# Performance work log

Hardware: AMD Instinct MI355X
Metric: run time of the kernel (lower is better)

The kernel has to match this reference:

```python
import jax, jax.numpy as jnp
import numpy as np

D_MODEL = 1024
NUM_HEADS = 16
DK = D_MODEL // NUM_HEADS


def setup_inputs() -> dict:
    key = jax.random.key(0)
    ks = jax.random.split(key, 9)
    s = 1.0 / np.sqrt(D_MODEL)
    x = jax.random.normal(ks[0], (4, 2048, D_MODEL), dtype=jnp.float32)
    Wq = jax.random.uniform(ks[1], (D_MODEL, D_MODEL), jnp.float32, -s, s)
    bq = jax.random.uniform(ks[2], (D_MODEL,), jnp.float32, -s, s)
    Wk = jax.random.uniform(ks[3], (D_MODEL, D_MODEL), jnp.float32, -s, s)
    bk = jax.random.uniform(ks[4], (D_MODEL,), jnp.float32, -s, s)
    Wv = jax.random.uniform(ks[5], (D_MODEL, D_MODEL), jnp.float32, -s, s)
    bv = jax.random.uniform(ks[6], (D_MODEL,), jnp.float32, -s, s)
    Wo = jax.random.uniform(ks[7], (D_MODEL, D_MODEL), jnp.float32, -s, s)
    bo = jax.random.uniform(ks[8], (D_MODEL,), jnp.float32, -s, s)
    return {"x": x, "Wq": Wq, "bq": bq, "Wk": Wk, "bk": bk,
            "Wv": Wv, "bv": bv, "Wo": Wo, "bo": bo}


def reference(x, Wq, bq, Wk, bk, Wv, bv, Wo, bo):
    B, S, _ = x.shape
    H, dk = NUM_HEADS, DK
    # QKV projections (nn.Linear: x @ W.T + b), split into heads -> [B,H,S,dk]
    q = (x @ Wq.T + bq).reshape(B, S, H, dk).transpose(0, 2, 1, 3)
    k = (x @ Wk.T + bk).reshape(B, S, H, dk).transpose(0, 2, 1, 3)
    v = (x @ Wv.T + bv).reshape(B, S, H, dk).transpose(0, 2, 1, 3)
    scores = jnp.einsum('bhqd,bhkd->bhqk', q, k) / jnp.sqrt(jnp.asarray(dk, x.dtype))
    causal = jnp.triu(jnp.ones((S, S), dtype=bool), k=1)  # True above diagonal
    scores = jnp.where(causal[None, None], -jnp.inf, scores)
    attn = jax.nn.softmax(scores, axis=-1)  # dropout p=0.0 -> identity
    out = jnp.einsum('bhqk,bhkd->bhqd', attn, v)
    out = out.transpose(0, 2, 1, 3).reshape(B, S, H * dk)
    return out @ Wo.T + bo
```

## Files before the change

### kernel.cpp

```cpp
#include <hip/hip_runtime.h>
#include <stdint.h>


#define D_MODEL 1024
#define NHEAD   16
#define DK      64
#define BATCH   4
#define SEQ     2048
#define MTOT    (BATCH*SEQ)

typedef unsigned short u16;
typedef unsigned int   u32;
typedef __bf16    bf16x8  __attribute__((ext_vector_type(8)));
typedef float     floatx4 __attribute__((ext_vector_type(4)));
typedef __fp16    fp16x2  __attribute__((ext_vector_type(2)));
typedef _Float16  half4_t __attribute__((ext_vector_type(4)));
typedef _Float16  half8_t __attribute__((ext_vector_type(8)));

__device__ __forceinline__ u16 f2bf(float f){
  union { float f; u32 u; } c; c.f = f;
  u32 x = c.u;
  x += 0x7fffu + ((x >> 16) & 1u);
  return (u16)(x >> 16);
}
__device__ __forceinline__ u32 pkh(float a, float b){
  union { fp16x2 h; u32 u; } c; c.h = __builtin_amdgcn_cvt_pkrtz(a, b); return c.u;
}
__device__ __forceinline__ uint4 pk8(const float* __restrict__ p){
  uint4 a = *(const uint4*)p;
  uint4 b = *(const uint4*)(p + 4);
  uint4 r;
  r.x = __builtin_amdgcn_perm(a.y, a.x, 0x07060302);
  r.y = __builtin_amdgcn_perm(a.w, a.z, 0x07060302);
  r.z = __builtin_amdgcn_perm(b.y, b.x, 0x07060302);
  r.w = __builtin_amdgcn_perm(b.w, b.z, 0x07060302);
  return r;
}
__device__ __forceinline__ void gload16(const void* g, void* l){
  __builtin_amdgcn_global_load_lds(
      (const __attribute__((address_space(1))) u32*)g,
      (__attribute__((address_space(3))) u32*)l, 16, 0, 0);
}

__global__ __launch_bounds__(256)
void conv4(const float* __restrict__ x,  u16* __restrict__ xb,
           const float* __restrict__ wq, const float* __restrict__ wk,
           const float* __restrict__ wv, u16* __restrict__ wb)
{
  const int b = blockIdx.x;
  const float* s; u16* d; size_t base;
  if (b < 4096)      { s = x;  d = xb;            base = (size_t)b * 2048; }
  else if (b < 4608) { s = wq; d = wb;            base = (size_t)(b-4096) * 2048; }
  else if (b < 5120) { s = wk; d = wb + (1u<<20); base = (size_t)(b-4608) * 2048; }
  else               { s = wv; d = wb + (2u<<20); base = (size_t)(b-5120) * 2048; }
  const size_t i = base + (size_t)threadIdx.x * 8;
  *(uint4*)(d + i) = pk8(s + i);
}

__global__ __launch_bounds__(256)
void conv1(const float* __restrict__ s, u16* __restrict__ d)
{
  const size_t i = ((size_t)blockIdx.x * 256 + threadIdx.x) * 8;
  *(uint4*)(d + i) = pk8(s + i);
}

template<int MODE>
__global__ __launch_bounds__(128, 2)
void gemm_bt(const u16* __restrict__ A, const u16* __restrict__ W,
             const float* __restrict__ bias, void* __restrict__ outv,
             float scale)
{
  __shared__ __align__(16) u16 As[128*32];
  __shared__ __align__(16) u16 Bs[64*32];

  const int t    = threadIdx.x;
  const int m0   = blockIdx.x * 128;
  const int n0   = blockIdx.y * 64;
  const int wid  = t >> 6, lane = t & 63;
  const int wr   = wid;
  const int quad = lane >> 4, l15 = lane & 15;

  const int rS = t >> 2;
  const int kS = (t & 3) * 8;

  const u16* Ap = A + (size_t)(m0 + rS)*D_MODEL + kS;
  const u16* Wp = W + (size_t)(n0 + rS)*D_MODEL + kS;

  floatx4 acc[4][4] = {};

  for (int k0 = 0; k0 < D_MODEL; k0 += 32) {
    __syncthreads();
    gload16(Ap + k0,               (char*)As + t*16);
    gload16(Ap + k0 + 32*D_MODEL,  (char*)As + 2048 + t*16);
    gload16(Ap + k0 + 64*D_MODEL,  (char*)As + 4096 + t*16);
    gload16(Ap + k0 + 96*D_MODEL,  (char*)As + 6144 + t*16);
    gload16(Wp + k0,               (char*)Bs + t*16);
    gload16(Wp + k0 + 32*D_MODEL,  (char*)Bs + 2048 + t*16);
    __syncthreads();

    bf16x8 af[4], bf[4];
#pragma unroll
    for (int i = 0; i < 4; ++i) {
      af[i] = *(const bf16x8*)&As[(wr*64 + i*16 + l15)*32 + quad*8];
      bf[i] = *(const bf16x8*)&Bs[(i*16 + l15)*32 + quad*8];
    }
#pragma unroll
    for (int mi = 0; mi < 4; ++mi)
#pragma unroll
      for (int nj = 0; nj < 4; ++nj) {
        if (MODE == 2)
          acc[mi][nj] = __builtin_amdgcn_mfma_f32_16x16x32_bf16(af[mi], bf[nj], acc[mi][nj], 0, 0, 0);
        else
          acc[mi][nj] = __builtin_amdgcn_mfma_f32_16x16x32_bf16(bf[nj], af[mi], acc[mi][nj], 0, 0, 0);
      }
  }

  if (MODE != 2) {
#pragma unroll
    for (int nj = 0; nj < 4; ++nj) {
      const int nb = n0 + nj*16 + quad*4;
      const float4 b4 = *(const float4*)(bias + nb);
#pragma unroll
      for (int mi = 0; mi < 4; ++mi) {
        const int m = m0 + wr*64 + mi*16 + l15;
        floatx4 d = acc[mi][nj];
        const float v0 = (d[0]+b4.x)*scale, v1 = (d[1]+b4.y)*scale;
        const float v2 = (d[2]+b4.z)*scale, v3 = (d[3]+b4.w)*scale;
        if (MODE == 0) {
          float4 s4 = make_float4(v0, v1, v2, v3);
          *(float4*)((float*)outv + (size_t)m*D_MODEL + nb) = s4;
        } else {
          const int b = m >> 11, s = m & 2047, h = nb >> 6, dd = nb & 63;
          u16* dst = (u16*)outv + ((((size_t)b*NHEAD + h)*SEQ + s) << 6) + dd;
          *(uint2*)dst = make_uint2(pkh(v0, v1), pkh(v2, v3));
        }
      }
    }
  } else {
#pragma unroll
    for (int nj = 0; nj < 4; ++nj) {
      const int n  = n0 + nj*16 + l15;
      const float bvv = bias[n];
      const int h = n >> 6, dd = n & 63;
#pragma unroll
      for (int mi = 0; mi < 4; ++mi) {
        const int mb = m0 + wr*64 + mi*16 + quad*4;
        const int b = mb >> 11, s = mb & 2047;
        floatx4 d = acc[mi][nj];
        u16* dst = (u16*)outv + (((size_t)b*NHEAD + h)*DK + dd)*SEQ + s;
        *(uint2*)dst = make_uint2(pkh(d[0]+bvv, d[1]+bvv), pkh(d[2]+bvv, d[3]+bvv));
      }
    }
  }
}

__global__ __launch_bounds__(256, 6)
void attn_fwd(const _Float16* __restrict__ Q, const _Float16* __restrict__ K,
              const _Float16* __restrict__ Vt, u16* __restrict__ O)
{
  __shared__ __align__(16) _Float16 Ks[64][72];
  __shared__ __align__(16) _Float16 Vs[64][72];

  const int bh   = blockIdx.x;
  const int pid  = blockIdx.y;
  const int t    = threadIdx.x;
  const int w    = t >> 6, lane = t & 63;
  const int quad = lane >> 4, l15 = lane & 15;
  const int sr = t >> 3, sc8 = (t & 7) * 8;
  const _Float16* Kb = K  + (size_t)bh * SEQ * DK;
  const _Float16* Vb = Vt + (size_t)bh * DK * SEQ;

#pragma unroll 1
  for (int item = 0; item < 2; ++item) {
    const int rblk = item ? pid : (SEQ/64 - 1 - pid);
    const int r0   = rblk * 64;
    const int qb   = r0 + w * 16;
    const int query = qb + l15;

    half8_t qf[2];
    {
      const _Float16* Qp = Q + ((size_t)bh * SEQ + query) * DK + quad * 8;
      qf[0] = *(const half8_t*)(Qp);
      qf[1] = *(const half8_t*)(Qp + 32);
    }

    float mrow = -1e30f, lpart = 0.f;
    floatx4 o[4] = {};

    const int jend = r0 + 64;
    for (int j0 = 0; j0 < jend; j0 += 64) {
      __syncthreads();
      *(uint4*)&Ks[sr     ][sc8] = *(const uint4*)(Kb + (size_t)(j0 + sr     )*DK + sc8);
      *(uint4*)&Ks[sr + 32][sc8] = *(const uint4*)(Kb + (size_t)(j0 + sr + 32)*DK + sc8);
      *(uint4*)&Vs[sr     ][sc8] = *(const uint4*)(Vb + (size_t)(sr     )*SEQ + j0 + sc8);
      *(uint4*)&Vs[sr + 32][sc8] = *(const uint4*)(Vb + (size_t)(sr + 32)*SEQ + j0 + sc8);
      __syncthreads();
      if (j0 > qb + 15) continue;
      const int ktmax = ((qb + 15 - j0) >> 4) + 1;

      floatx4 st[4];
#pragma unroll
      for (int kt = 0; kt < 4; ++kt) {
        if (kt < ktmax) {
          half8_t a0 = *(const half8_t*)&Ks[kt*16 + l15][quad*8];
          half8_t a1 = *(const half8_t*)&Ks[kt*16 + l15][32 + quad*8];
          floatx4 s = {};
          s = __builtin_amdgcn_mfma_f32_16x16x32_f16(a0, qf[0], s, 0, 0, 0);
          s = __builtin_amdgcn_mfma_f32_16x16x32_f16(a1, qf[1], s, 0, 0, 0);
          st[kt] = s;
        }
      }
#pragma unroll
      for (int kt = 0; kt < 4; ++kt) {
        if (kt < ktmax && j0 + kt*16 + 15 > qb) {
#pragma unroll
          for (int r = 0; r < 4; ++r)
            if (j0 + kt*16 + quad*4 + r > query) st[kt][r] = -1e30f;
        }
      }
      float m0 = -1e30f;
#pragma unroll
      for (int kt = 0; kt < 4; ++kt)
        if (kt < ktmax)
          m0 = fmaxf(m0, fmaxf(fmaxf(st[kt][0], st[kt][1]), fmaxf(st[kt][2], st[kt][3])));
      m0 = fmaxf(m0, __shfl_xor(m0, 16));
      m0 = fmaxf(m0, __shfl_xor(m0, 32));
      const float mn    = fmaxf(mrow, m0);
      const float alpha = exp2f(mrow - mn);
      mrow = mn;
      lpart *= alpha;
      half4_t pf[4];
#pragma unroll
      for (int kt = 0; kt < 4; ++kt) {
        if (kt < ktmax) {
          const float p0 = exp2f(st[kt][0] - mn), p1 = exp2f(st[kt][1] - mn);
          const float p2 = exp2f(st[kt][2] - mn), p3 = exp2f(st[kt][3] - mn);
          lpart += (p0 + p1) + (p2 + p3);
          union { half4_t h; uint2 u; } pc;
          pc.u = make_uint2(pkh(p0, p1), pkh(p2, p3));
          pf[kt] = pc.h;
        }
      }
#pragma unroll
      for (int dt = 0; dt < 4; ++dt) {
        o[dt][0] *= alpha; o[dt][1] *= alpha; o[dt][2] *= alpha; o[dt][3] *= alpha;
      }
#pragma unroll
      for (int dt = 0; dt < 4; ++dt)
#pragma unroll
        for (int kt = 0; kt < 4; ++kt) {
          if (kt < ktmax) {
            half4_t vf = *(const half4_t*)&Vs[dt*16 + l15][kt*16 + quad*4];
            o[dt] = __builtin_amdgcn_mfma_f32_16x16x16f16(vf, pf[kt], o[dt], 0, 0, 0);
          }
        }
    }

    float l = lpart;
    l += __shfl_xor(l, 16);
    l += __shfl_xor(l, 32);
    const float inv = 1.0f / l;
    const int b = bh >> 4, h = bh & 15;
    u16* Op = O + ((size_t)(b * SEQ + query)) * D_MODEL + h * DK + quad * 4;
#pragma unroll
    for (int dt = 0; dt < 4; ++dt) {
      u32 lo = ((u32)f2bf(o[dt][1] * inv) << 16) | f2bf(o[dt][0] * inv);
      u32 hi = ((u32)f2bf(o[dt][3] * inv) << 16) | f2bf(o[dt][2] * inv);
      *(uint2*)(Op + dt * 16) = make_uint2(lo, hi);
    }
  }
}

extern "C" void kernel_launch(void* const* d_in, const int* in_sizes, int n_in,
                              void* d_out, int out_size, void* d_ws, size_t ws_size,
                              hipStream_t stream)
{
  const float* x  = (const float*)d_in[0];
  const float* Wq = (const float*)d_in[1];
  const float* bq = (const float*)d_in[2];
  const float* Wk = (const float*)d_in[3];
  const float* bk = (const float*)d_in[4];
  const float* Wv = (const float*)d_in[5];
  const float* bv = (const float*)d_in[6];
  const float* Wo = (const float*)d_in[7];
  const float* bo = (const float*)d_in[8];

  const size_t tsz = (size_t)MTOT * D_MODEL;
  u16* Qw  = (u16*)d_ws;
  u16* Kw  = Qw + tsz;
  u16* Vtw = Kw + tsz;
  u16* S3  = Vtw + tsz;
  u16* WB  = (u16*)d_out;

  conv4<<<4096 + 3*512, 256, 0, stream>>>(x, S3, Wq, Wk, Wv, WB);

  dim3 gg(MTOT/128, D_MODEL/64);
  gemm_bt<1><<<gg, 128, 0, stream>>>(S3, WB,            bq, Qw,  0.18033688f);
  gemm_bt<1><<<gg, 128, 0, stream>>>(S3, WB + (1u<<20), bk, Kw,  1.0f);
  gemm_bt<2><<<gg, 128, 0, stream>>>(S3, WB + (2u<<20), bv, Vtw, 1.0f);

  attn_fwd<<<dim3(BATCH*NHEAD, SEQ/128), 256, 0, stream>>>(
      (const _Float16*)Qw, (const _Float16*)Kw, (const _Float16*)Vtw, S3);

  conv1<<<512, 256, 0, stream>>>(Wo, Qw);
  gemm_bt<0><<<gg, 128, 0, stream>>>(S3, Qw, bo, d_out, 1.0f);
}
```

Before: 322.6 us.

## Process both causal query blocks in one pass over shared K/V tiles

```diff
diff --git a/kernel.cpp b/kernel.cpp
--- a/kernel.cpp
+++ b/kernel.cpp
@@ -154,7 +154,72 @@
   }
 }
 
-__global__ __launch_bounds__(256, 6)
+__device__ __forceinline__ void attn_tile(
+    const _Float16 (*Ks)[72], const _Float16 (*Vs)[72],
+    int j0, int qb, int query, int quad, int l15,
+    const half8_t* qf, float& mrow, float& lpart, floatx4* o)
+{
+  const int ktmax = ((qb + 15 - j0) >> 4) + 1;
+
+  floatx4 st[4];
+#pragma unroll
+  for (int kt = 0; kt < 4; ++kt) {
+    if (kt < ktmax) {
+      half8_t a0 = *(const half8_t*)&Ks[kt*16 + l15][quad*8];
+      half8_t a1 = *(const half8_t*)&Ks[kt*16 + l15][32 + quad*8];
+      floatx4 s = {};
+      s = __builtin_amdgcn_mfma_f32_16x16x32_f16(a0, qf[0], s, 0, 0, 0);
+      s = __builtin_amdgcn_mfma_f32_16x16x32_f16(a1, qf[1], s, 0, 0, 0);
+      st[kt] = s;
+    }
+  }
+#pragma unroll
+  for (int kt = 0; kt < 4; ++kt) {
+    if (kt < ktmax && j0 + kt*16 + 15 > qb) {
+#pragma unroll
+      for (int r = 0; r < 4; ++r)
+        if (j0 + kt*16 + quad*4 + r > query) st[kt][r] = -1e30f;
+    }
+  }
+  float m0 = -1e30f;
+#pragma unroll
+  for (int kt = 0; kt < 4; ++kt)
+    if (kt < ktmax)
+      m0 = fmaxf(m0, fmaxf(fmaxf(st[kt][0], st[kt][1]), fmaxf(st[kt][2], st[kt][3])));
+  m0 = fmaxf(m0, __shfl_xor(m0, 16));
+  m0 = fmaxf(m0, __shfl_xor(m0, 32));
+  const float mn    = fmaxf(mrow, m0);
+  const float alpha = exp2f(mrow - mn);
+  mrow = mn;
+  lpart *= alpha;
+  half4_t pf[4];
+#pragma unroll
+  for (int kt = 0; kt < 4; ++kt) {
+    if (kt < ktmax) {
+      const float p0 = exp2f(st[kt][0] - mn), p1 = exp2f(st[kt][1] - mn);
+      const float p2 = exp2f(st[kt][2] - mn), p3 = exp2f(st[kt][3] - mn);
+      lpart += (p0 + p1) + (p2 + p3);
+      union { half4_t h; uint2 u; } pc;
+      pc.u = make_uint2(pkh(p0, p1), pkh(p2, p3));
+      pf[kt] = pc.h;
+    }
+  }
+#pragma unroll
+  for (int dt = 0; dt < 4; ++dt) {
+    o[dt][0] *= alpha; o[dt][1] *= alpha; o[dt][2] *= alpha; o[dt][3] *= alpha;
+  }
+#pragma unroll
+  for (int dt = 0; dt < 4; ++dt)
+#pragma unroll
+    for (int kt = 0; kt < 4; ++kt) {
+      if (kt < ktmax) {
+        half4_t vf = *(const half4_t*)&Vs[dt*16 + l15][kt*16 + quad*4];
+        o[dt] = __builtin_amdgcn_mfma_f32_16x16x16f16(vf, pf[kt], o[dt], 0, 0, 0);
+      }
+    }
+}
+
+__global__ __launch_bounds__(256, 4)
 void attn_fwd(const _Float16* __restrict__ Q, const _Float16* __restrict__ K,
               const _Float16* __restrict__ Vt, u16* __restrict__ O)
 {
@@ -170,102 +235,65 @@
   const _Float16* Kb = K  + (size_t)bh * SEQ * DK;
   const _Float16* Vb = Vt + (size_t)bh * DK * SEQ;
 
+  const int rblk0 = 31 - pid;
+  const int rblk1 = pid;
+  const int qb0 = rblk0*64 + w*16, q0 = qb0 + l15;
+  const int qb1 = rblk1*64 + w*16, q1 = qb1 + l15;
+
+  half8_t qf0[2], qf1[2];
+  {
+    const _Float16* Qp0 = Q + ((size_t)bh * SEQ + q0) * DK + quad * 8;
+    qf0[0] = *(const half8_t*)(Qp0);
+    qf0[1] = *(const half8_t*)(Qp0 + 32);
+    const _Float16* Qp1 = Q + ((size_t)bh * SEQ + q1) * DK + quad * 8;
+    qf1[0] = *(const half8_t*)(Qp1);
+    qf1[1] = *(const half8_t*)(Qp1 + 32);
+  }
+
+  float mrow0 = -1e30f, lpart0 = 0.f;
+  float mrow1 = -1e30f, lpart1 = 0.f;
+  floatx4 o0[4] = {};
+  floatx4 o1[4] = {};
+
+  const int jend = rblk0*64 + 64;
 #pragma unroll 1
-  for (int item = 0; item < 2; ++item) {
-    const int rblk = item ? pid : (SEQ/64 - 1 - pid);
-    const int r0   = rblk * 64;
-    const int qb   = r0 + w * 16;
-    const int query = qb + l15;
-
-    half8_t qf[2];
-    {
-      const _Float16* Qp = Q + ((size_t)bh * SEQ + query) * DK + quad * 8;
-      qf[0] = *(const half8_t*)(Qp);
-      qf[1] = *(const half8_t*)(Qp + 32);
-    }
-
-    float mrow = -1e30f, lpart = 0.f;
-    floatx4 o[4] = {};
-
-    const int jend = r0 + 64;
-    for (int j0 = 0; j0 < jend; j0 += 64) {
-      __syncthreads();
-      *(uint4*)&Ks[sr     ][sc8] = *(const uint4*)(Kb + (size_t)(j0 + sr     )*DK + sc8);
-      *(uint4*)&Ks[sr + 32][sc8] = *(const uint4*)(Kb + (size_t)(j0 + sr + 32)*DK + sc8);
-      *(uint4*)&Vs[sr     ][sc8] = *(const uint4*)(Vb + (size_t)(sr     )*SEQ + j0 + sc8);
-      *(uint4*)&Vs[sr + 32][sc8] = *(const uint4*)(Vb + (size_t)(sr + 32)*SEQ + j0 + sc8);
-      __syncthreads();
-      if (j0 > qb + 15) continue;
-      const int ktmax = ((qb + 15 - j0) >> 4) + 1;
-
-      floatx4 st[4];
-#pragma unroll
-      for (int kt = 0; kt < 4; ++kt) {
-        if (kt < ktmax) {
-          half8_t a0 = *(const half8_t*)&Ks[kt*16 + l15][quad*8];
-          half8_t a1 = *(const half8_t*)&Ks[kt*16 + l15][32 + quad*8];
-          floatx4 s = {};
-          s = __builtin_amdgcn_mfma_f32_16x16x32_f16(a0, qf[0], s, 0, 0, 0);
-          s = __builtin_amdgcn_mfma_f32_16x16x32_f16(a1, qf[1], s, 0, 0, 0);
-          st[kt] = s;
-        }
-      }
-#pragma unroll
-      for (int kt = 0; kt < 4; ++kt) {
-        if (kt < ktmax && j0 + kt*16 + 15 > qb) {
-#pragma unroll
-          for (int r = 0; r < 4; ++r)
-            if (j0 + kt*16 + quad*4 + r > query) st[kt][r] = -1e30f;
-        }
-      }
-      float m0 = -1e30f;
-#pragma unroll
-      for (int kt = 0; kt < 4; ++kt)
-        if (kt < ktmax)
-          m0 = fmaxf(m0, fmaxf(fmaxf(st[kt][0], st[kt][1]), fmaxf(st[kt][2], st[kt][3])));
-      m0 = fmaxf(m0, __shfl_xor(m0, 16));
-      m0 = fmaxf(m0, __shfl_xor(m0, 32));
-      const float mn    = fmaxf(mrow, m0);
-      const float alpha = exp2f(mrow - mn);
-      mrow = mn;
-      lpart *= alpha;
-      half4_t pf[4];
-#pragma unroll
-      for (int kt = 0; kt < 4; ++kt) {
-        if (kt < ktmax) {
-          const float p0 = exp2f(st[kt][0] - mn), p1 = exp2f(st[kt][1] - mn);
-          const float p2 = exp2f(st[kt][2] - mn), p3 = exp2f(st[kt][3] - mn);
-          lpart += (p0 + p1) + (p2 + p3);
-          union { half4_t h; uint2 u; } pc;
-          pc.u = make_uint2(pkh(p0, p1), pkh(p2, p3));
-          pf[kt] = pc.h;
-        }
-      }
-#pragma unroll
-      for (int dt = 0; dt < 4; ++dt) {
-        o[dt][0] *= alpha; o[dt][1] *= alpha; o[dt][2] *= alpha; o[dt][3] *= alpha;
-      }
-#pragma unroll
-      for (int dt = 0; dt < 4; ++dt)
-#pragma unroll
-        for (int kt = 0; kt < 4; ++kt) {
-          if (kt < ktmax) {
-            half4_t vf = *(const half4_t*)&Vs[dt*16 + l15][kt*16 + quad*4];
-            o[dt] = __builtin_amdgcn_mfma_f32_16x16x16f16(vf, pf[kt], o[dt], 0, 0, 0);
-          }
-        }
-    }
-
-    float l = lpart;
+  for (int j0 = 0; j0 < jend; j0 += 64) {
+    __syncthreads();
+    *(uint4*)&Ks[sr     ][sc8] = *(const uint4*)(Kb + (size_t)(j0 + sr     )*DK + sc8);
+    *(uint4*)&Ks[sr + 32][sc8] = *(const uint4*)(Kb + (size_t)(j0 + sr + 32)*DK + sc8);
+    *(uint4*)&Vs[sr     ][sc8] = *(const uint4*)(Vb + (size_t)(sr     )*SEQ + j0 + sc8);
+    *(uint4*)&Vs[sr + 32][sc8] = *(const uint4*)(Vb + (size_t)(sr + 32)*SEQ + j0 + sc8);
+    __syncthreads();
+    if (j0 <= qb0 + 15)
+      attn_tile(Ks, Vs, j0, qb0, q0, quad, l15, qf0, mrow0, lpart0, o0);
+    if (j0 <= qb1 + 15)
+      attn_tile(Ks, Vs, j0, qb1, q1, quad, l15, qf1, mrow1, lpart1, o1);
+  }
+
+  const int b = bh >> 4, h = bh & 15;
+  {
+    float l = lpart0;
     l += __shfl_xor(l, 16);
     l += __shfl_xor(l, 32);
     const float inv = 1.0f / l;
-    const int b = bh >> 4, h = bh & 15;
-    u16* Op = O + ((size_t)(b * SEQ + query)) * D_MODEL + h * DK + quad * 4;
+    u16* Op = O + ((size_t)(b * SEQ + q0)) * D_MODEL + h * DK + quad * 4;
 #pragma unroll
     for (int dt = 0; dt < 4; ++dt) {
-      u32 lo = ((u32)f2bf(o[dt][1] * inv) << 16) | f2bf(o[dt][0] * inv);
-      u32 hi = ((u32)f2bf(o[dt][3] * inv) << 16) | f2bf(o[dt][2] * inv);
+      u32 lo = ((u32)f2bf(o0[dt][1] * inv) << 16) | f2bf(o0[dt][0] * inv);
+      u32 hi = ((u32)f2bf(o0[dt][3] * inv) << 16) | f2bf(o0[dt][2] * inv);
+      *(uint2*)(Op + dt * 16) = make_uint2(lo, hi);
+    }
+  }
+  {
+    float l = lpart1;
+    l += __shfl_xor(l, 16);
+    l += __shfl_xor(l, 32);
+    const float inv = 1.0f / l;
+    u16* Op = O + ((size_t)(b * SEQ + q1)) * D_MODEL + h * DK + quad * 4;
+#pragma unroll
+    for (int dt = 0; dt < 4; ++dt) {
+      u32 lo = ((u32)f2bf(o1[dt][1] * inv) << 16) | f2bf(o1[dt][0] * inv);
+      u32 hi = ((u32)f2bf(o1[dt][3] * inv) << 16) | f2bf(o1[dt][2] * inv);
       *(uint2*)(Op + dt * 16) = make_uint2(lo, hi);
     }
   }
```

Result: faster. 315.1 us (-2.3%).
